# Optimization experiments

Measured on AMD Instinct MI355X. Metric: run time of the kernel, lower is better.

Reference implementation:

```python
import jax, jax.numpy as jnp
import numpy as np

NEG_MASK = -10000.0  # matches torch.triu(full(..., -10000.0), 1) additive causal mask


def setup_inputs() -> dict:
    key = jax.random.key(0)
    qkv = jax.random.normal(key, (2, 2048, 3, 16, 64), dtype=jnp.float32)
    return {"qkv": qkv}


def reference(qkv):
    # qkv: [B, S, 3, H, D]
    seqlen = qkv.shape[1]
    q = qkv[:, :, 0]  # [B, S, H, D]
    k = qkv[:, :, 1]
    v = qkv[:, :, 2]
    softmax_scale = q.shape[-1] ** (-0.5)
    # scores: [B, H, T, S]
    scores = jnp.einsum('bthd,bshd->bhts', q, k * softmax_scale)
    # additive causal mask (strict upper triangle gets -10000.0)
    causal_mask = jnp.triu(jnp.full((seqlen, seqlen), NEG_MASK, dtype=scores.dtype), 1)
    scores = scores + causal_mask
    attention = jax.nn.softmax(scores, axis=-1)
    # dropout p=0.0 -> identity
    output = jnp.einsum('bhts,bshd->bthd', attention, v)  # [B, T, H, D]
    return output
```

## Files before the change

### kernel.cpp

```cpp
#include <hip/hip_runtime.h>
#include <hip/hip_bf16.h>


#define SEQ   2048
#define HEADS 16

typedef __attribute__((ext_vector_type(8))) _Float16 half8v;
typedef __attribute__((ext_vector_type(4))) float f32x4;
typedef __attribute__((ext_vector_type(4))) int   int4v;

static __device__ __forceinline__ int pkrtz(float a, float b) {
    return __builtin_bit_cast(int, __builtin_amdgcn_cvt_pkrtz(a, b));
}

__global__ __launch_bounds__(512, 6)
void attn_f16(const float* __restrict__ qkv, float* __restrict__ out) {
    const int n   = blockIdx.x;
    const int bh  = n & 31;
    const int idx = n >> 5;
    int jq;
    if      (idx <  8) jq = 31 - idx;
    else if (idx < 16) jq = idx - 8;
    else if (idx < 24) jq = 39 - idx;
    else               jq = idx - 16;
    const int q0 = jq * 64;
    const int b = bh >> 4, h = bh & 15;
    const int NT = jq + 1;

    const int tid  = threadIdx.x;
    const int lane = tid & 63;
    const int w    = tid >> 6;
    const int rg   = w >> 1;
    const int ks   = w & 1;
    const int l15  = lane & 15, lhi = lane >> 4;
    const int qbase = q0 + rg * 16;
    const int qrow  = qbase + l15;
    const int wqmax = qbase + 15;

    __shared__ __align__(16) char lds[2][16384];

    const float QSCALE = 0.125f * 1.44269504088896340736f;
    half8v qf[2];
    #pragma unroll
    for (int c = 0; c < 2; ++c) {
        const float* p = qkv + (size_t)(b * SEQ + qrow) * 3072 + h * 64 + c * 32 + lhi * 8;
        const float4 f0 = *(const float4*)p;
        const float4 f1 = *(const float4*)(p + 4);
        int4v u;
        u[0] = pkrtz(f0.x * QSCALE, f0.y * QSCALE);
        u[1] = pkrtz(f0.z * QSCALE, f0.w * QSCALE);
        u[2] = pkrtz(f1.x * QSCALE, f1.y * QSCALE);
        u[3] = pkrtz(f1.z * QSCALE, f1.w * QSCALE);
        qf[c] = __builtin_bit_cast(half8v, u);
    }

    const f32x4 fzero = {0.f, 0.f, 0.f, 0.f};
    f32x4 acc[4];
    #pragma unroll
    for (int dt = 0; dt < 4; ++dt) acc[dt] = fzero;
    float lsum = 0.f;

    const int skey = tid >> 3;
    const int sd0  = (tid & 7) * 8;
    const int kwb  = skey * 128 + ((sd0 * 2) ^ ((skey & 7) << 4));
    const int vk0  = (tid >> 4) * 2;
    const int vd0  = (tid & 15) * 4;
    const int kk   = vk0 & 31, kcS = vk0 >> 5;
    const int i0   = (kk & 3) + ((kk >> 4) & 1) * 4;
    const int grp  = (kk >> 2) & 3;
    const int vswz = (((kk >> 3) & 1) << 6);

    const float* kgp = qkv + (size_t)b * SEQ * 3072 + (size_t)(HEADS + h) * 64 + sd0;
    const float* vgp = qkv + (size_t)b * SEQ * 3072 + (size_t)(2 * HEADS + h) * 64 + vd0;

    {
        const float* kp = kgp + (size_t)skey * 3072;
        const float4 a0 = *(const float4*)kp, a1 = *(const float4*)(kp + 4);
        int4v ku;
        ku[0] = pkrtz(a0.x, a0.y); ku[1] = pkrtz(a0.z, a0.w);
        ku[2] = pkrtz(a1.x, a1.y); ku[3] = pkrtz(a1.z, a1.w);
        *(int4v*)(lds[0] + kwb) = ku;
        const float* vp = vgp + (size_t)vk0 * 3072;
        const float4 v0 = *(const float4*)vp;
        const float4 v1 = *(const float4*)(vp + 3072);
        const float* f0 = (const float*)&v0;
        const float* f1 = (const float*)&v1;
        #pragma unroll
        for (int dd = 0; dd < 4; ++dd) {
            const int d  = vd0 + dd, dt = d >> 4;
            const int vb = 8192 + kcS * 4096
                         + ((dt * 1024 + (grp * 16 + (d & 15)) * 16 + i0 * 2)
                            ^ (vswz | ((dt & 1) << 4) | (((dt >> 1) & 1) << 5)));
            *(int*)(lds[0] + vb) = pkrtz(f0[dd], f1[dd]);
        }
    }
    __syncthreads();

    int cur = 0;
    for (int t = 0; t < NT; ++t) {
        const int c0 = t * 64 + ks * 32;
        if (c0 <= wqmax) {
            const char* buf = lds[cur];
            const bool interior = (c0 + 32 <= qbase);
            int4v pu;
            float ps = 0.f;
            #pragma unroll
            for (int kt = 0; kt < 2; ++kt) {
                const int row = ks * 32 + kt * 16 + l15;
                const int bx  = row * 128;
                const int sw  = (l15 & 7) << 4;
                const half8v k0 = *(const half8v*)(buf + bx + ((lhi * 16) ^ sw));
                const half8v k1 = *(const half8v*)(buf + bx + ((64 + lhi * 16) ^ sw));
                __builtin_amdgcn_s_setprio(1);
                f32x4 d = fzero;
                d = __builtin_amdgcn_mfma_f32_16x16x32_f16(k0, qf[0], d, 0, 0, 0);
                d = __builtin_amdgcn_mfma_f32_16x16x32_f16(k1, qf[1], d, 0, 0, 0);
                __builtin_amdgcn_s_setprio(0);
                const int kb = c0 + kt * 16 + lhi * 4;
                float e[4];
                #pragma unroll
                for (int r = 0; r < 4; ++r)
                    e[r] = (interior || (kb + r <= qrow))
                         ? __builtin_amdgcn_exp2f(d[r]) : 0.0f;
                pu[kt * 2 + 0] = pkrtz(e[0], e[1]);
                pu[kt * 2 + 1] = pkrtz(e[2], e[3]);
                ps += (e[0] + e[1]) + (e[2] + e[3]);
            }
            lsum += ps;
            const half8v pa = __builtin_bit_cast(half8v, pu);

            __builtin_amdgcn_s_setprio(1);
            #pragma unroll
            for (int dt = 0; dt < 4; ++dt) {
                const int rb = 8192 + ks * 4096
                             + ((dt * 1024 + lane * 16)
                                ^ (((dt & 1) << 4) | (((dt >> 1) & 1) << 5) | (((lane >> 5) & 1) << 6)));
                const half8v vf = *(const half8v*)(buf + rb);
                acc[dt] = __builtin_amdgcn_mfma_f32_16x16x32_f16(pa, vf, acc[dt], 0, 0, 0);
            }
            __builtin_amdgcn_s_setprio(0);
        }
        if (t + 1 < NT) {
            char* obuf = lds[cur ^ 1];
            const float* kp = kgp + (size_t)((t + 1) * 64 + skey) * 3072;
            const float4 a0 = *(const float4*)kp, a1 = *(const float4*)(kp + 4);
            int4v ku;
            ku[0] = pkrtz(a0.x, a0.y); ku[1] = pkrtz(a0.z, a0.w);
            ku[2] = pkrtz(a1.x, a1.y); ku[3] = pkrtz(a1.z, a1.w);
            *(int4v*)(obuf + kwb) = ku;
            const float* vp = vgp + (size_t)((t + 1) * 64 + vk0) * 3072;
            const float4 v0 = *(const float4*)vp;
            const float4 v1 = *(const float4*)(vp + 3072);
            const float* f0 = (const float*)&v0;
            const float* f1 = (const float*)&v1;
            #pragma unroll
            for (int dd = 0; dd < 4; ++dd) {
                const int d  = vd0 + dd, dt = d >> 4;
                const int vb = 8192 + kcS * 4096
                             + ((dt * 1024 + (grp * 16 + (d & 15)) * 16 + i0 * 2)
                                ^ (vswz | ((dt & 1) << 4) | (((dt >> 1) & 1) << 5)));
                *(int*)(obuf + vb) = pkrtz(f0[dd], f1[dd]);
            }
        }
        __syncthreads();
        cur ^= 1;
    }

    float s = lsum;
    s += __shfl_xor(s, 16);
    s += __shfl_xor(s, 32);

    float* accm = (float*)lds[0];
    float* lsm  = (float*)lds[1];
    if (ks == 1) {
        float* a = accm + (rg * 64 + lane) * 16;
        #pragma unroll
        for (int dt = 0; dt < 4; ++dt)
            #pragma unroll
            for (int r = 0; r < 4; ++r)
                a[dt * 4 + r] = acc[dt][r];
        lsm[rg * 64 + lane] = s;
    }
    __syncthreads();
    if (ks == 0) {
        const float* a = accm + (rg * 64 + lane) * 16;
        const float stot = s + lsm[rg * 64 + lane];
        #pragma unroll
        for (int dt = 0; dt < 4; ++dt)
            #pragma unroll
            for (int r = 0; r < 4; ++r)
                acc[dt][r] += a[dt * 4 + r];
        #pragma unroll
        for (int r = 0; r < 4; ++r) {
            const float sr  = __shfl(stot, lhi * 4 + r);
            const float inv = 1.0f / sr;
            const int orow  = qbase + lhi * 4 + r;
            float* op = out + ((size_t)(b * SEQ + orow) * HEADS + h) * 64 + l15;
            #pragma unroll
            for (int dt = 0; dt < 4; ++dt)
                op[dt * 16] = acc[dt][r] * inv;
        }
    }
}

extern "C" void kernel_launch(void* const* d_in, const int* in_sizes, int n_in,
                              void* d_out, int out_size, void* d_ws, size_t ws_size,
                              hipStream_t stream) {
    const float* qkv = (const float*)d_in[0];
    float* out = (float*)d_out;
    dim3 grid(1024);
    dim3 block(512);
    attn_f16<<<grid, block, 0, stream>>>(qkv, out);
}
```

Baseline: 115.1 us.

## Prefetch next K/V tile early and compute row sums via MFMA

Global loads for the next K/V tile are now issued at the top of each iteration, before the QK/PV compute, so their latency overlaps the MFMAs instead of stalling afterwards. The per-lane scalar softmax row-sum adds are replaced by an extra MFMA that multiplies P by a ones vector, which yields row sums already in the accumulator layout and removes the final shuffles. The epilogue LDS layout is padded (stride 17 and 5) to avoid bank conflicts. This costs extra registers for the held float4 values and one more MFMA per tile, which may affect occupancy at the 6-wave launch bound.

```diff
diff --git a/kernel.cpp b/kernel.cpp
--- a/kernel.cpp
+++ b/kernel.cpp
@@ -54,11 +54,15 @@
         qf[c] = __builtin_bit_cast(half8v, u);
     }
 
+    half8v vones;
+    #pragma unroll
+    for (int i = 0; i < 8; ++i) vones[i] = (_Float16)1.0f;
+
     const f32x4 fzero = {0.f, 0.f, 0.f, 0.f};
     f32x4 acc[4];
     #pragma unroll
     for (int dt = 0; dt < 4; ++dt) acc[dt] = fzero;
-    float lsum = 0.f;
+    f32x4 accl = fzero;
 
     const int skey = tid >> 3;
     const int sd0  = (tid & 7) * 8;
@@ -99,11 +103,22 @@
     int cur = 0;
     for (int t = 0; t < NT; ++t) {
         const int c0 = t * 64 + ks * 32;
+
+        float4 ka0, ka1, va0, va1;
+        const bool have_next = (t + 1 < NT);
+        if (have_next) {
+            const float* kp = kgp + (size_t)((t + 1) * 64 + skey) * 3072;
+            ka0 = *(const float4*)kp;
+            ka1 = *(const float4*)(kp + 4);
+            const float* vp = vgp + (size_t)((t + 1) * 64 + vk0) * 3072;
+            va0 = *(const float4*)vp;
+            va1 = *(const float4*)(vp + 3072);
+        }
+
         if (c0 <= wqmax) {
             const char* buf = lds[cur];
             const bool interior = (c0 + 32 <= qbase);
             int4v pu;
-            float ps = 0.f;
             #pragma unroll
             for (int kt = 0; kt < 2; ++kt) {
                 const int row = ks * 32 + kt * 16 + l15;
@@ -124,9 +139,7 @@
                          ? __builtin_amdgcn_exp2f(d[r]) : 0.0f;
                 pu[kt * 2 + 0] = pkrtz(e[0], e[1]);
                 pu[kt * 2 + 1] = pkrtz(e[2], e[3]);
-                ps += (e[0] + e[1]) + (e[2] + e[3]);
             }
-            lsum += ps;
             const half8v pa = __builtin_bit_cast(half8v, pu);
 
             __builtin_amdgcn_s_setprio(1);
@@ -138,21 +151,18 @@
                 const half8v vf = *(const half8v*)(buf + rb);
                 acc[dt] = __builtin_amdgcn_mfma_f32_16x16x32_f16(pa, vf, acc[dt], 0, 0, 0);
             }
+            accl = __builtin_amdgcn_mfma_f32_16x16x32_f16(pa, vones, accl, 0, 0, 0);
             __builtin_amdgcn_s_setprio(0);
         }
-        if (t + 1 < NT) {
+
+        if (have_next) {
             char* obuf = lds[cur ^ 1];
-            const float* kp = kgp + (size_t)((t + 1) * 64 + skey) * 3072;
-            const float4 a0 = *(const float4*)kp, a1 = *(const float4*)(kp + 4);
             int4v ku;
-            ku[0] = pkrtz(a0.x, a0.y); ku[1] = pkrtz(a0.z, a0.w);
-            ku[2] = pkrtz(a1.x, a1.y); ku[3] = pkrtz(a1.z, a1.w);
+            ku[0] = pkrtz(ka0.x, ka0.y); ku[1] = pkrtz(ka0.z, ka0.w);
+            ku[2] = pkrtz(ka1.x, ka1.y); ku[3] = pkrtz(ka1.z, ka1.w);
             *(int4v*)(obuf + kwb) = ku;
-            const float* vp = vgp + (size_t)((t + 1) * 64 + vk0) * 3072;
-            const float4 v0 = *(const float4*)vp;
-            const float4 v1 = *(const float4*)(vp + 3072);
-            const float* f0 = (const float*)&v0;
-            const float* f1 = (const float*)&v1;
+            const float* f0 = (const float*)&va0;
+            const float* f1 = (const float*)&va1;
             #pragma unroll
             for (int dd = 0; dd < 4; ++dd) {
                 const int d  = vd0 + dd, dt = d >> 4;
@@ -166,25 +176,25 @@
         cur ^= 1;
     }
 
-    float s = lsum;
-    s += __shfl_xor(s, 16);
-    s += __shfl_xor(s, 32);
-
-    float* accm = (float*)lds[0];
-    float* lsm  = (float*)lds[1];
+    char* base  = &lds[0][0];
+    float* accm = (float*)base;
+    float* lsm4 = (float*)(base + 17408);
+    const int slot = rg * 64 + lane;
     if (ks == 1) {
-        float* a = accm + (rg * 64 + lane) * 16;
+        float* a = accm + slot * 17;
         #pragma unroll
         for (int dt = 0; dt < 4; ++dt)
             #pragma unroll
             for (int r = 0; r < 4; ++r)
                 a[dt * 4 + r] = acc[dt][r];
-        lsm[rg * 64 + lane] = s;
+        float* l4 = lsm4 + slot * 5;
+        #pragma unroll
+        for (int r = 0; r < 4; ++r) l4[r] = accl[r];
     }
     __syncthreads();
     if (ks == 0) {
-        const float* a = accm + (rg * 64 + lane) * 16;
-        const float stot = s + lsm[rg * 64 + lane];
+        const float* a  = accm + slot * 17;
+        const float* l4 = lsm4 + slot * 5;
         #pragma unroll
         for (int dt = 0; dt < 4; ++dt)
             #pragma unroll
@@ -192,8 +202,7 @@
                 acc[dt][r] += a[dt * 4 + r];
         #pragma unroll
         for (int r = 0; r < 4; ++r) {
-            const float sr  = __shfl(stot, lhi * 4 + r);
-            const float inv = 1.0f / sr;
+            const float inv = 1.0f / (accl[r] + l4[r]);
             const int orow  = qbase + lhi * 4 + r;
             float* op = out + ((size_t)(b * SEQ + orow) * HEADS + h) * 64 + l15;
             #pragma unroll
```

Result: slower. 138.5 us (+20.4%).
